# Kernel tuning notes

Hardware: AMD Instinct MI355X
Metric: run time of the kernel (lower is better)

## Reference

```python
import math
import jax, jax.numpy as jnp
import numpy as np

DIM_IN = 2048
DIM_OUT = 2048
BLOCK = 128
N_BLOCKS = 256
SPARSITY = 0.1
BATCH = 8192


def setup_inputs() -> dict:
    key = jax.random.key(0)
    k1, k2, k3, k4, k5 = jax.random.split(key, 5)
    x = jax.random.normal(k1, (BATCH, DIM_IN), dtype=jnp.float32)
    weight = jax.random.normal(k2, (DIM_IN, DIM_OUT), dtype=jnp.float32) * (1.0 / math.sqrt(DIM_IN))
    bias = jax.random.normal(k3, (DIM_OUT,), dtype=jnp.float32) * 0.01
    gate_w = jax.random.normal(k4, (DIM_IN, N_BLOCKS), dtype=jnp.float32) * (1.0 / math.sqrt(DIM_IN))
    gate_b = jax.random.normal(k5, (N_BLOCKS,), dtype=jnp.float32) * 0.01
    return {"x": x, "weight": weight, "bias": bias, "gate_w": gate_w, "gate_b": gate_b}


def _sparsify1d(g):
    # k-th largest kept per row; threshold, mask, renormalize (Sparsify1D)
    n = g.shape[-1]
    k = int(math.ceil(SPARSITY * n))
    topval = jax.lax.top_k(g, k)[0][:, -1:]          # (B, 1) k-th largest value
    res = jnp.where(g >= topval, g, jnp.zeros_like(g))
    return res / (jnp.sum(res, axis=-1, keepdims=True) / n)


def reference(x, weight, bias, gate_w, gate_b):
    B = x.shape[0]
    s = DIM_IN // BLOCK                               # 16 block-rows/cols
    # gate network: Linear -> Sparsify1D
    g = _sparsify1d(x @ gate_w + gate_b)              # (B, s*s)
    gb = g.reshape(B, s, s)                           # (B, s_in, s_out)
    xb = x.reshape(B, s, BLOCK)                       # (B, s_in, block)
    Wb = weight.reshape(s, BLOCK, s, BLOCK)           # (s_in, block, s_out, block)
    # gated block matrix-vector multiply:
    # y[b,q,n] = sum_{p,m} g[b,p,q] * x[b,p,m] * W[p,m,q,n]
    y = jnp.einsum('bpq,bpm,pmqn->bqn', gb, xb, Wb)
    return y.reshape(B, DIM_OUT) + bias
```

## Files before the change

### kernel.cpp

```cpp
#include <hip/hip_runtime.h>
#include <hip/hip_bf16.h>
#include <stdint.h>

#define BATCH  8192
#define DIN    2048
#define DOUT   2048
#define NB     256
#define KSEL   26
#define GDELTA 1e-4f

typedef __attribute__((ext_vector_type(2))) float f32x2;
typedef __attribute__((ext_vector_type(4))) float f32x4;
typedef __attribute__((ext_vector_type(16))) float f32x16;
typedef __attribute__((ext_vector_type(8))) __bf16 bf16x8;
typedef __attribute__((ext_vector_type(8))) unsigned short u16x8;
typedef __attribute__((ext_vector_type(4))) unsigned short u16x4;

__device__ __forceinline__ float bf2f(unsigned short u){
  union { unsigned int i; float f; } v; v.i = ((unsigned int)u) << 16; return v.f;
}
__device__ __forceinline__ unsigned short f2bf(float f){
  union { float f; unsigned int i; } v; v.f = f;
  unsigned int x = v.i;
  return (unsigned short)((x + 0x7FFFu + ((x >> 16) & 1u)) >> 16);
}
__device__ __forceinline__ unsigned short f2bf_c(float f){
  __bf16 b = (__bf16)f;
  union { __bf16 b; unsigned short u; } v; v.b = b; return v.u;
}

__global__ __launch_bounds__(256) void conv_wt(const float* __restrict__ w, unsigned short* __restrict__ wt)
{
  __shared__ float tl[64][65];
  const int k0 = blockIdx.x * 64;
  const int n0 = blockIdx.y * 64;
  const int c  = threadIdx.x & 63;
  const int r4 = threadIdx.x >> 6;
  #pragma unroll
  for (int i = 0; i < 16; i++){
    const int r = r4 * 16 + i;
    tl[r][c] = w[(size_t)(k0 + r) * DOUT + n0 + c];
  }
  __syncthreads();
  #pragma unroll
  for (int i = 0; i < 16; i++){
    const int n = r4 * 16 + i;
    wt[(size_t)(n0 + n) * DIN + k0 + c] = f2bf(tl[c][n]);
  }
}

__global__ __launch_bounds__(256) void conv_gwt(const float* __restrict__ gw,
    unsigned short* __restrict__ ghiT, unsigned short* __restrict__ gloT)
{
  __shared__ float tl[64][65];
  const int k0 = blockIdx.x * 64;
  const int n0 = blockIdx.y * 64;
  const int c  = threadIdx.x & 63;
  const int r4 = threadIdx.x >> 6;
  #pragma unroll
  for (int i = 0; i < 16; i++){
    const int r = r4 * 16 + i;
    tl[r][c] = gw[(size_t)(k0 + r) * NB + n0 + c];
  }
  __syncthreads();
  #pragma unroll
  for (int i = 0; i < 16; i++){
    const int n = r4 * 16 + i;
    const float v = tl[c][n];
    const unsigned short h = f2bf_c(v);
    ghiT[(size_t)(n0 + n) * DIN + k0 + c] = h;
    gloT[(size_t)(n0 + n) * DIN + k0 + c] = f2bf_c(v - bf2f(h));
  }
}

__global__ __launch_bounds__(256) void gate_v2(
    const float* __restrict__ x,
    const unsigned short* __restrict__ ghiT,
    const unsigned short* __restrict__ gloT,
    float* __restrict__ part,
    unsigned short* __restrict__ xb)
{
  __shared__ unsigned short Axh[64][64], Axl[64][64];
  __shared__ unsigned short Bgh[128][64], Bgl[128][64];

  const int b0   = blockIdx.x * 64;
  const int c0   = blockIdx.y * 128;
  const int ks   = blockIdx.z;
  const int k0   = ks * 1024;
  const int t    = threadIdx.x;
  const int lane = t & 63;
  const int wv   = t >> 6;
  const int bw   = wv & 1;
  const int cw   = wv >> 1;
  const int l15  = lane & 15;
  const int l4   = lane >> 4;
  const bool emit = (blockIdx.y == 0);

  const int ar = t >> 2;
  const int ak = (t & 3) * 16;
  const int br = t >> 1;
  const int bk = (t & 1) * 32;

  f32x4 acc[2][4];
  #pragma unroll
  for (int m = 0; m < 2; m++)
    #pragma unroll
    for (int n = 0; n < 4; n++) acc[m][n] = (f32x4)0.0f;

  int aoff[2][2], boff[2][4];
  #pragma unroll
  for (int ksi = 0; ksi < 2; ksi++){
    const int chunk = ksi * 4 + l4;
    #pragma unroll
    for (int m = 0; m < 2; m++){
      const int row = bw * 32 + m * 16 + l15;
      aoff[ksi][m] = row * 64 + ((chunk ^ (row & 7)) << 3);
    }
    #pragma unroll
    for (int n = 0; n < 4; n++){
      const int row = cw * 64 + n * 16 + l15;
      boff[ksi][n] = row * 64 + ((chunk ^ (row & 7)) << 3);
    }
  }

  f32x4 xa[4];
  u16x8 gh[4], glo[4];

  auto LOAD = [&](int kb){
    const float* xp = &x[(size_t)(b0 + ar) * DIN + kb + ak];
    #pragma unroll
    for (int j = 0; j < 4; j++) xa[j] = ((const f32x4*)xp)[j];
    const unsigned short* hp = &ghiT[(size_t)(c0 + br) * DIN + kb + bk];
    const unsigned short* lp = &gloT[(size_t)(c0 + br) * DIN + kb + bk];
    #pragma unroll
    for (int j = 0; j < 4; j++){ gh[j] = ((const u16x8*)hp)[j]; glo[j] = ((const u16x8*)lp)[j]; }
  };

  auto WRITE = [&](int kb){
    const int asw = ar & 7;
    #pragma unroll
    for (int h = 0; h < 2; h++){
      u16x8 hi, lo;
      #pragma unroll
      for (int j = 0; j < 8; j++){
        const float v = xa[h * 2 + (j >> 2)][j & 3];
        const __bf16 hb = (__bf16)v;
        union { __bf16 b; unsigned short u; } uh; uh.b = hb;
        hi[j] = uh.u;
        lo[j] = f2bf_c(v - (float)hb);
      }
      const int c8 = (((ak >> 3) + h) ^ asw) << 3;
      *(u16x8*)&Axh[ar][c8] = hi;
      *(u16x8*)&Axl[ar][c8] = lo;
      if (emit) *(u16x8*)&xb[(size_t)(b0 + ar) * DIN + kb + ak + h * 8] = hi;
    }
    const int bsw = br & 7;
    #pragma unroll
    for (int j = 0; j < 4; j++){
      const int c8 = (((bk >> 3) + j) ^ bsw) << 3;
      *(u16x8*)&Bgh[br][c8] = gh[j];
      *(u16x8*)&Bgl[br][c8] = glo[j];
    }
  };

  const unsigned short* Ah0 = &Axh[0][0];
  const unsigned short* Al0 = &Axl[0][0];
  const unsigned short* Bh0 = &Bgh[0][0];
  const unsigned short* Bl0 = &Bgl[0][0];

  LOAD(k0);
  #pragma unroll 1
  for (int s = 0; s < 16; s++){
    const int kb = k0 + s * 64;
    __syncthreads();
    WRITE(kb);
    __syncthreads();
    if (s < 15) LOAD(kb + 64);
    #pragma unroll
    for (int ksi = 0; ksi < 2; ksi++){
      bf16x8 ah[2], al[2], bh[4], bl[4];
      #pragma unroll
      for (int m = 0; m < 2; m++){
        ah[m] = *(const bf16x8*)&Ah0[aoff[ksi][m]];
        al[m] = *(const bf16x8*)&Al0[aoff[ksi][m]];
      }
      #pragma unroll
      for (int n = 0; n < 4; n++){
        bh[n] = *(const bf16x8*)&Bh0[boff[ksi][n]];
        bl[n] = *(const bf16x8*)&Bl0[boff[ksi][n]];
      }
      #pragma unroll
      for (int m = 0; m < 2; m++)
        #pragma unroll
        for (int n = 0; n < 4; n++){
          acc[m][n] = __builtin_amdgcn_mfma_f32_16x16x32_bf16(ah[m], bh[n], acc[m][n], 0, 0, 0);
          acc[m][n] = __builtin_amdgcn_mfma_f32_16x16x32_bf16(al[m], bh[n], acc[m][n], 0, 0, 0);
          acc[m][n] = __builtin_amdgcn_mfma_f32_16x16x32_bf16(ah[m], bl[n], acc[m][n], 0, 0, 0);
        }
    }
  }

  float* dst = part + (size_t)ks * BATCH * NB;
  #pragma unroll
  for (int m = 0; m < 2; m++){
    const int brow = b0 + bw * 32 + m * 16 + l4 * 4;
    #pragma unroll
    for (int n = 0; n < 4; n++){
      const int ccol = c0 + cw * 64 + n * 16 + l15;
      #pragma unroll
      for (int r = 0; r < 4; r++)
        dst[(size_t)(brow + r) * NB + ccol] = acc[m][n][r];
    }
  }
}

__global__ __launch_bounds__(256) void topk(float* __restrict__ part,
    const float* __restrict__ gb, int* __restrict__ flags)
{
  const int lane = threadIdx.x & 63;
  const int row  = blockIdx.x * 4 + (threadIdx.x >> 6);
  f32x4* p0 = (f32x4*)&part[(size_t)row * NB];
  const f32x4* p1 = (const f32x4*)&part[(size_t)(BATCH + row) * NB];
  const f32x4* gbv = (const f32x4*)gb;
  f32x4 v = p0[lane] + p1[lane] + gbv[lane];

  const float NEG = -3.402823466e38f;
  float w0 = v[0], w1 = v[1], w2 = v[2], w3 = v[3];
  float thr = 0.f, nxt = 0.f;
  for (int it = 0; it < KSEL + 1; it++){
    float lm = fmaxf(fmaxf(w0, w1), fmaxf(w2, w3));
    float wm = lm;
    #pragma unroll
    for (int off = 32; off; off >>= 1) wm = fmaxf(wm, __shfl_xor(wm, off, 64));
    unsigned long long ball = __ballot(lm == wm);
    int first = __ffsll(ball) - 1;
    if (lane == first){
      if      (w0 == wm) w0 = NEG;
      else if (w1 == wm) w1 = NEG;
      else if (w2 == wm) w2 = NEG;
      else               w3 = NEG;
    }
    if (it < KSEL) thr = wm; else nxt = wm;
  }
  if (lane == 0) flags[row] = (thr - nxt < GDELTA) ? 1 : 0;

  float s = 0.f;
  #pragma unroll
  for (int j = 0; j < 4; j++) s += (v[j] >= thr) ? v[j] : 0.f;
  #pragma unroll
  for (int off = 32; off; off >>= 1) s += __shfl_xor(s, off, 64);
  const float d = s * (1.0f / NB);
  f32x4 o;
  #pragma unroll
  for (int j = 0; j < 4; j++) o[j] = (v[j] >= thr) ? v[j] / d : 0.f;
  p0[lane] = o;
}

__global__ __launch_bounds__(256) void refine(
    const float* __restrict__ x, const float* __restrict__ gw,
    const float* __restrict__ gb, const int* __restrict__ flags,
    float* __restrict__ part)
{
  const int lane = threadIdx.x & 63;
  const int row  = blockIdx.x * 4 + (threadIdx.x >> 6);
  if (!flags[row]) return;

  f32x4 acc0 = (f32x4)0.f, acc1 = (f32x4)0.f;
  const float* xp = &x[(size_t)row * DIN];
  #pragma unroll 8
  for (int k = 0; k < 1024; k++){
    const float xv = xp[k];
    const f32x4 wv = *(const f32x4*)&gw[(size_t)k * NB + lane * 4];
    #pragma unroll
    for (int j = 0; j < 4; j++) acc0[j] = fmaf(xv, wv[j], acc0[j]);
  }
  #pragma unroll 8
  for (int k = 1024; k < 2048; k++){
    const float xv = xp[k];
    const f32x4 wv = *(const f32x4*)&gw[(size_t)k * NB + lane * 4];
    #pragma unroll
    for (int j = 0; j < 4; j++) acc1[j] = fmaf(xv, wv[j], acc1[j]);
  }
  const f32x4 gbv = *(const f32x4*)&gb[lane * 4];
  f32x4 v;
  #pragma unroll
  for (int j = 0; j < 4; j++) v[j] = acc0[j] + acc1[j] + gbv[j];

  const float NEG = -3.402823466e38f;
  float w0 = v[0], w1 = v[1], w2 = v[2], w3 = v[3];
  float thr = 0.f;
  for (int it = 0; it < KSEL; it++){
    float lm = fmaxf(fmaxf(w0, w1), fmaxf(w2, w3));
    float wm = lm;
    #pragma unroll
    for (int off = 32; off; off >>= 1) wm = fmaxf(wm, __shfl_xor(wm, off, 64));
    unsigned long long ball = __ballot(lm == wm);
    int first = __ffsll(ball) - 1;
    if (lane == first){
      if      (w0 == wm) w0 = NEG;
      else if (w1 == wm) w1 = NEG;
      else if (w2 == wm) w2 = NEG;
      else               w3 = NEG;
    }
    thr = wm;
  }
  float s = 0.f;
  #pragma unroll
  for (int j = 0; j < 4; j++) s += (v[j] >= thr) ? v[j] : 0.f;
  #pragma unroll
  for (int off = 32; off; off >>= 1) s += __shfl_xor(s, off, 64);
  const float d = s * (1.0f / NB);
  f32x4 o;
  #pragma unroll
  for (int j = 0; j < 4; j++) o[j] = (v[j] >= thr) ? v[j] / d : 0.f;
  *(f32x4*)&part[(size_t)row * NB + lane * 4] = o;
}

__global__ __launch_bounds__(256) void main_v2(
    const unsigned short* __restrict__ xb,
    const unsigned short* __restrict__ wt,
    const float* __restrict__ g,
    const float* __restrict__ bias,
    float* __restrict__ out)
{
  __shared__ unsigned short XA[128][64];
  __shared__ unsigned short WB[128][64];
  __shared__ float gl[128 * 17];

  const int f  = blockIdx.x;
  const int q  = f >> 6;
  const int b0 = ((f & 7) * 8 + ((f >> 3) & 7)) * 128;
  const int t    = threadIdx.x;
  const int lane = t & 63;
  const int wid  = t >> 6;
  const int wr   = (wid >> 1) * 64;
  const int wc   = (wid & 1) * 64;
  const int l15  = lane & 15;
  const int l4   = lane >> 4;

  for (int e = t; e < 128 * 16; e += 256){
    const int r = e >> 4, p = e & 15;
    gl[r * 17 + p] = g[(size_t)(b0 + r) * NB + p * 16 + q];
  }

  f32x4 acc[4][4];
  #pragma unroll
  for (int m = 0; m < 4; m++)
    #pragma unroll
    for (int n = 0; n < 4; n++) acc[m][n] = (f32x4)0.0f;

  const int row_s = t >> 1;
  const int half  = t & 1;
  const int kk    = half * 32;

  int aoff[2][4], boff[2][4];
  #pragma unroll
  for (int ksi = 0; ksi < 2; ksi++){
    const int chunk = ksi * 4 + l4;
    #pragma unroll
    for (int m = 0; m < 4; m++){
      const int row = wr + m * 16 + l15;
      aoff[ksi][m] = row * 64 + ((chunk ^ (row & 7)) << 3);
    }
    #pragma unroll
    for (int n = 0; n < 4; n++){
      const int row = wc + n * 16 + l15;
      boff[ksi][n] = row * 64 + ((chunk ^ (row & 7)) << 3);
    }
  }

  u16x8 ax[4], bx[4];
  auto LOAD = [&](int kb){
    const unsigned short* asrc = &xb[(size_t)(b0 + row_s) * DIN + kb + kk];
    const unsigned short* bsrc = &wt[(size_t)(q * 128 + row_s) * DIN + kb + kk];
    #pragma unroll
    for (int j = 0; j < 4; j++){ ax[j] = ((const u16x8*)asrc)[j]; bx[j] = ((const u16x8*)bsrc)[j]; }
  };
  auto WRITE = [&](int p){
    const float gate = gl[row_s * 17 + p];
    const int sw = row_s & 7;
    #pragma unroll
    for (int j = 0; j < 4; j++){
      u16x8 o;
      #pragma unroll
      for (int i = 0; i < 8; i++) o[i] = f2bf_c(bf2f(ax[j][i]) * gate);
      const int c8 = ((half * 4 + j) ^ sw) << 3;
      *(u16x8*)&XA[row_s][c8] = o;
      *(u16x8*)&WB[row_s][c8] = bx[j];
    }
  };

  const unsigned short* A0 = &XA[0][0];
  const unsigned short* B0 = &WB[0][0];

  LOAD(0);
  #pragma unroll 1
  for (int kp = 0; kp < 32; kp++){
    __syncthreads();
    WRITE(kp >> 1);
    __syncthreads();
    if (kp < 31) LOAD((kp + 1) * 64);
    #pragma unroll
    for (int ksi = 0; ksi < 2; ksi++){
      bf16x8 a[4], b[4];
      #pragma unroll
      for (int m = 0; m < 4; m++) a[m] = *(const bf16x8*)&A0[aoff[ksi][m]];
      #pragma unroll
      for (int n = 0; n < 4; n++) b[n] = *(const bf16x8*)&B0[boff[ksi][n]];
      #pragma unroll
      for (int m = 0; m < 4; m++)
        #pragma unroll
        for (int n = 0; n < 4; n++)
          acc[m][n] = __builtin_amdgcn_mfma_f32_16x16x32_bf16(a[m], b[n], acc[m][n], 0, 0, 0);
    }
  }

  #pragma unroll
  for (int n = 0; n < 4; n++){
    const int col = q * 128 + wc + n * 16 + l15;
    const float bv = bias[col];
    #pragma unroll
    for (int m = 0; m < 4; m++){
      #pragma unroll
      for (int r = 0; r < 4; r++){
        const int row = b0 + wr + m * 16 + l4 * 4 + r;
        out[(size_t)row * DOUT + col] = acc[m][n][r] + bv;
      }
    }
  }
}

extern "C" void kernel_launch(void* const* d_in, const int* in_sizes, int n_in,
                              void* d_out, int out_size, void* d_ws, size_t ws_size,
                              hipStream_t stream)
{
  const float* x    = (const float*)d_in[0];
  const float* w    = (const float*)d_in[1];
  const float* bias = (const float*)d_in[2];
  const float* gw   = (const float*)d_in[3];
  const float* gb   = (const float*)d_in[4];
  float* out = (float*)d_out;

  char* wsb = (char*)d_ws;
  float*          part = (float*)wsb;
  unsigned short* xbb  = (unsigned short*)(wsb + (size_t)16 * 1024 * 1024);
  unsigned short* ghiT = (unsigned short*)(wsb + (size_t)48 * 1024 * 1024);
  unsigned short* gloT = (unsigned short*)(wsb + (size_t)49 * 1024 * 1024);
  int*            flg  = (int*)           (wsb + (size_t)50 * 1024 * 1024);
  unsigned short* wtb  = (unsigned short*)(wsb + (size_t)48 * 1024 * 1024);

  conv_gwt <<<dim3(DIN / 64, NB / 64), 256, 0, stream>>>(gw, ghiT, gloT);
  gate_v2  <<<dim3(BATCH / 64, 2, 2), 256, 0, stream>>>(x, ghiT, gloT, part, xbb);
  topk     <<<BATCH / 4, 256, 0, stream>>>(part, gb, flg);
  refine   <<<BATCH / 4, 256, 0, stream>>>(x, gw, gb, flg, part);
  conv_wt  <<<dim3(DIN / 64, DOUT / 64), 256, 0, stream>>>(w, wtb);
  main_v2  <<<1024, 256, 0, stream>>>(xbb, wtb, part, bias, out);
}
```

Before: 257.0 us.

## Pre-tile swizzled bf16 operands and stream via global_load_lds double buffering

The weight, gate-weight and bf16 x conversions now write tiles in a pre-swizzled, tile-contiguous layout. This lets the gate and main GEMMs load shared-memory tiles directly with global_load_lds into double buffers, with no register staging. The main kernel no longer scales x by the gate before the MFMA. It accumulates each 128-wide input block into a partial accumulator and applies the per-row gate in fp32 afterward, which removes the per-element convert/multiply/convert and one barrier per step. The cost is doubled LDS usage and extra accumulator registers, which may lower occupancy. The gate GEMM tile shape also changes to 128x64.

Result: slower. 288.3 us (+12.2%).

```diff
diff --git a/kernel.cpp b/kernel.cpp
--- a/kernel.cpp
+++ b/kernel.cpp
@@ -9,27 +9,26 @@
 #define KSEL   26
 #define GDELTA 1e-4f
 
-typedef __attribute__((ext_vector_type(2))) float f32x2;
 typedef __attribute__((ext_vector_type(4))) float f32x4;
-typedef __attribute__((ext_vector_type(16))) float f32x16;
 typedef __attribute__((ext_vector_type(8))) __bf16 bf16x8;
 typedef __attribute__((ext_vector_type(8))) unsigned short u16x8;
-typedef __attribute__((ext_vector_type(4))) unsigned short u16x4;
 
 __device__ __forceinline__ float bf2f(unsigned short u){
   union { unsigned int i; float f; } v; v.i = ((unsigned int)u) << 16; return v.f;
-}
-__device__ __forceinline__ unsigned short f2bf(float f){
-  union { float f; unsigned int i; } v; v.f = f;
-  unsigned int x = v.i;
-  return (unsigned short)((x + 0x7FFFu + ((x >> 16) & 1u)) >> 16);
 }
 __device__ __forceinline__ unsigned short f2bf_c(float f){
   __bf16 b = (__bf16)f;
   union { __bf16 b; unsigned short u; } v; v.b = b; return v.u;
 }
-
-__global__ __launch_bounds__(256) void conv_wt(const float* __restrict__ w, unsigned short* __restrict__ wt)
+__device__ __forceinline__ void gload16(const unsigned short* g, unsigned short* l){
+  __builtin_amdgcn_global_load_lds(
+      (const __attribute__((address_space(1))) void*)g,
+      (__attribute__((address_space(3))) void*)l, 16, 0, 0);
+}
+
+
+__global__ __launch_bounds__(256) void conv_wt2(const float* __restrict__ w,
+                                                unsigned short* __restrict__ wtt)
 {
   __shared__ float tl[64][65];
   const int k0 = blockIdx.x * 64;
@@ -42,171 +41,182 @@
     tl[r][c] = w[(size_t)(k0 + r) * DOUT + n0 + c];
   }
   __syncthreads();
-  #pragma unroll
-  for (int i = 0; i < 16; i++){
-    const int n = r4 * 16 + i;
-    wt[(size_t)(n0 + n) * DIN + k0 + c] = f2bf(tl[c][n]);
-  }
-}
-
-__global__ __launch_bounds__(256) void conv_gwt(const float* __restrict__ gw,
-    unsigned short* __restrict__ ghiT, unsigned short* __restrict__ gloT)
+  const int n  = threadIdx.x & 63;
+  const int cp = threadIdx.x >> 6;
+  const int gn = n0 + n;
+  const size_t base = ((size_t)(gn >> 7) * 32 + (k0 >> 6)) * 8192 + (size_t)(gn & 127) * 64;
+  const int sw = gn & 7;
+  #pragma unroll
+  for (int u = 0; u < 2; u++){
+    const int cc = cp * 2 + u;
+    u16x8 o;
+    #pragma unroll
+    for (int j = 0; j < 8; j++) o[j] = f2bf_c(tl[cc * 8 + j][n]);
+    *(u16x8*)&wtt[base + ((cc ^ sw) << 3)] = o;
+  }
+}
+
+__global__ __launch_bounds__(256) void conv_gwt2(const float* __restrict__ gw,
+    unsigned short* __restrict__ ght, unsigned short* __restrict__ glt)
 {
   __shared__ float tl[64][65];
   const int k0 = blockIdx.x * 64;
-  const int n0 = blockIdx.y * 64;
+  const int c0 = blockIdx.y * 64;
   const int c  = threadIdx.x & 63;
   const int r4 = threadIdx.x >> 6;
   #pragma unroll
   for (int i = 0; i < 16; i++){
     const int r = r4 * 16 + i;
-    tl[r][c] = gw[(size_t)(k0 + r) * NB + n0 + c];
+    tl[r][c] = gw[(size_t)(k0 + r) * NB + c0 + c];
   }
   __syncthreads();
-  #pragma unroll
-  for (int i = 0; i < 16; i++){
-    const int n = r4 * 16 + i;
-    const float v = tl[c][n];
-    const unsigned short h = f2bf_c(v);
-    ghiT[(size_t)(n0 + n) * DIN + k0 + c] = h;
-    gloT[(size_t)(n0 + n) * DIN + k0 + c] = f2bf_c(v - bf2f(h));
-  }
-}
-
-__global__ __launch_bounds__(256) void gate_v2(
+  const int n  = threadIdx.x & 63;
+  const int cp = threadIdx.x >> 6;
+  const size_t base = ((size_t)(c0 >> 6) * 32 + (k0 >> 6)) * 4096 + (size_t)n * 64;
+  const int sw = n & 7;
+  #pragma unroll
+  for (int u = 0; u < 2; u++){
+    const int cc = cp * 2 + u;
+    u16x8 hi, lo;
+    #pragma unroll
+    for (int j = 0; j < 8; j++){
+      const float v = tl[cc * 8 + j][n];
+      const __bf16 hb = (__bf16)v;
+      union { __bf16 b; unsigned short u; } uh; uh.b = hb;
+      hi[j] = uh.u;
+      lo[j] = f2bf_c(v - (float)hb);
+    }
+    const int off = (cc ^ sw) << 3;
+    *(u16x8*)&ght[base + off] = hi;
+    *(u16x8*)&glt[base + off] = lo;
+  }
+}
+
+__global__ __launch_bounds__(256) void gate_v3(
     const float* __restrict__ x,
-    const unsigned short* __restrict__ ghiT,
-    const unsigned short* __restrict__ gloT,
+    const unsigned short* __restrict__ ght,
+    const unsigned short* __restrict__ glt,
     float* __restrict__ part,
-    unsigned short* __restrict__ xb)
-{
-  __shared__ unsigned short Axh[64][64], Axl[64][64];
-  __shared__ unsigned short Bgh[128][64], Bgl[128][64];
-
-  const int b0   = blockIdx.x * 64;
-  const int c0   = blockIdx.y * 128;
-  const int ks   = blockIdx.z;
-  const int k0   = ks * 1024;
+    unsigned short* __restrict__ xbt)
+{
+  __shared__ unsigned short Axh[128 * 64], Axl[128 * 64];
+  __shared__ unsigned short Bh[2][64 * 64], Bl[2][64 * 64];
+
+  const int b0   = blockIdx.x * 128;
+  const int ct   = blockIdx.y;
+  const int z    = blockIdx.z;
+  const int ks0  = z * 16;
   const int t    = threadIdx.x;
   const int lane = t & 63;
-  const int wv   = t >> 6;
-  const int bw   = wv & 1;
-  const int cw   = wv >> 1;
+  const int wid  = t >> 6;
+  const int bw   = wid & 1;
+  const int cw   = wid >> 1;
   const int l15  = lane & 15;
   const int l4   = lane >> 4;
   const bool emit = (blockIdx.y == 0);
 
-  const int ar = t >> 2;
-  const int ak = (t & 3) * 16;
-  const int br = t >> 1;
-  const int bk = (t & 1) * 32;
-
-  f32x4 acc[2][4];
-  #pragma unroll
-  for (int m = 0; m < 2; m++)
-    #pragma unroll
-    for (int n = 0; n < 4; n++) acc[m][n] = (f32x4)0.0f;
-
-  int aoff[2][2], boff[2][4];
+  const int ar  = t >> 1;
+  const int ah4 = (t & 1) * 4;
+
+  f32x4 acc[4][2];
+  #pragma unroll
+  for (int m = 0; m < 4; m++)
+    #pragma unroll
+    for (int n = 0; n < 2; n++) acc[m][n] = (f32x4)0.0f;
+
+  int aoff[2][4], boff[2][2];
   #pragma unroll
   for (int ksi = 0; ksi < 2; ksi++){
     const int chunk = ksi * 4 + l4;
     #pragma unroll
-    for (int m = 0; m < 2; m++){
-      const int row = bw * 32 + m * 16 + l15;
+    for (int m = 0; m < 4; m++){
+      const int row = bw * 64 + m * 16 + l15;
       aoff[ksi][m] = row * 64 + ((chunk ^ (row & 7)) << 3);
     }
     #pragma unroll
-    for (int n = 0; n < 4; n++){
-      const int row = cw * 64 + n * 16 + l15;
+    for (int n = 0; n < 2; n++){
+      const int row = cw * 32 + n * 16 + l15;
       boff[ksi][n] = row * 64 + ((chunk ^ (row & 7)) << 3);
     }
   }
 
-  f32x4 xa[4];
-  u16x8 gh[4], glo[4];
-
-  auto LOAD = [&](int kb){
-    const float* xp = &x[(size_t)(b0 + ar) * DIN + kb + ak];
-    #pragma unroll
-    for (int j = 0; j < 4; j++) xa[j] = ((const f32x4*)xp)[j];
-    const unsigned short* hp = &ghiT[(size_t)(c0 + br) * DIN + kb + bk];
-    const unsigned short* lp = &gloT[(size_t)(c0 + br) * DIN + kb + bk];
-    #pragma unroll
-    for (int j = 0; j < 4; j++){ gh[j] = ((const u16x8*)hp)[j]; glo[j] = ((const u16x8*)lp)[j]; }
+  f32x4 xr[8];
+  auto LOADX = [&](int s){
+    const float* xp = &x[(size_t)(b0 + ar) * DIN + (size_t)(ks0 + s) * 64 + ah4 * 8];
+    #pragma unroll
+    for (int j = 0; j < 8; j++) xr[j] = ((const f32x4*)xp)[j];
   };
-
-  auto WRITE = [&](int kb){
-    const int asw = ar & 7;
-    #pragma unroll
-    for (int h = 0; h < 2; h++){
+  auto GLOADB = [&](int bb, int s){
+    const size_t base = ((size_t)ct * 32 + (ks0 + s)) * 4096;
+    #pragma unroll
+    for (int i = 0; i < 2; i++){
+      const int slot = (wid * 2 + i) * 512;
+      gload16(ght + base + slot + lane * 8, &Bh[bb][slot]);
+      gload16(glt + base + slot + lane * 8, &Bl[bb][slot]);
+    }
+  };
+  auto WRITEA = [&](int s){
+    const int sw = ar & 7;
+    const size_t gb = ((size_t)(b0 >> 7) * 32 + (ks0 + s)) * 8192 + (size_t)ar * 64;
+    #pragma unroll
+    for (int j = 0; j < 4; j++){
       u16x8 hi, lo;
       #pragma unroll
-      for (int j = 0; j < 8; j++){
-        const float v = xa[h * 2 + (j >> 2)][j & 3];
+      for (int e = 0; e < 8; e++){
+        const float v = xr[j * 2 + (e >> 2)][e & 3];
         const __bf16 hb = (__bf16)v;
         union { __bf16 b; unsigned short u; } uh; uh.b = hb;
-        hi[j] = uh.u;
-        lo[j] = f2bf_c(v - (float)hb);
+        hi[e] = uh.u;
+        lo[e] = f2bf_c(v - (float)hb);
       }
-      const int c8 = (((ak >> 3) + h) ^ asw) << 3;
-      *(u16x8*)&Axh[ar][c8] = hi;
-      *(u16x8*)&Axl[ar][c8] = lo;
-      if (emit) *(u16x8*)&xb[(size_t)(b0 + ar) * DIN + kb + ak + h * 8] = hi;
-    }
-    const int bsw = br & 7;
-    #pragma unroll
-    for (int j = 0; j < 4; j++){
-      const int c8 = (((bk >> 3) + j) ^ bsw) << 3;
-      *(u16x8*)&Bgh[br][c8] = gh[j];
-      *(u16x8*)&Bgl[br][c8] = glo[j];
+      const int c8 = ((ah4 + j) ^ sw) << 3;
+      *(u16x8*)&Axh[ar * 64 + c8] = hi;
+      *(u16x8*)&Axl[ar * 64 + c8] = lo;
+      if (emit) *(u16x8*)&xbt[gb + c8] = hi;
     }
   };
 
-  const unsigned short* Ah0 = &Axh[0][0];
-  const unsigned short* Al0 = &Axl[0][0];
-  const unsigned short* Bh0 = &Bgh[0][0];
-  const unsigned short* Bl0 = &Bgl[0][0];
-
-  LOAD(k0);
+  GLOADB(0, 0);
+  LOADX(0);
+  int buf = 0;
   #pragma unroll 1
   for (int s = 0; s < 16; s++){
-    const int kb = k0 + s * 64;
     __syncthreads();
-    WRITE(kb);
+    WRITEA(s);
     __syncthreads();
-    if (s < 15) LOAD(kb + 64);
+    if (s < 15){ GLOADB(buf ^ 1, s + 1); LOADX(s + 1); }
     #pragma unroll
     for (int ksi = 0; ksi < 2; ksi++){
-      bf16x8 ah[2], al[2], bh[4], bl[4];
-      #pragma unroll
-      for (int m = 0; m < 2; m++){
-        ah[m] = *(const bf16x8*)&Ah0[aoff[ksi][m]];
-        al[m] = *(const bf16x8*)&Al0[aoff[ksi][m]];
+      bf16x8 ah[4], al[4], bh[2], bl[2];
+      #pragma unroll
+      for (int m = 0; m < 4; m++){
+        ah[m] = *(const bf16x8*)&Axh[aoff[ksi][m]];
+        al[m] = *(const bf16x8*)&Axl[aoff[ksi][m]];
       }
       #pragma unroll
-      for (int n = 0; n < 4; n++){
-        bh[n] = *(const bf16x8*)&Bh0[boff[ksi][n]];
-        bl[n] = *(const bf16x8*)&Bl0[boff[ksi][n]];
+      for (int n = 0; n < 2; n++){
+        bh[n] = *(const bf16x8*)&Bh[buf][boff[ksi][n]];
+        bl[n] = *(const bf16x8*)&Bl[buf][boff[ksi][n]];
       }
       #pragma unroll
-      for (int m = 0; m < 2; m++)
+      for (int m = 0; m < 4; m++)
         #pragma unroll
-        for (int n = 0; n < 4; n++){
+        for (int n = 0; n < 2; n++){
           acc[m][n] = __builtin_amdgcn_mfma_f32_16x16x32_bf16(ah[m], bh[n], acc[m][n], 0, 0, 0);
           acc[m][n] = __builtin_amdgcn_mfma_f32_16x16x32_bf16(al[m], bh[n], acc[m][n], 0, 0, 0);
           acc[m][n] = __builtin_amdgcn_mfma_f32_16x16x32_bf16(ah[m], bl[n], acc[m][n], 0, 0, 0);
         }
     }
-  }
-
-  float* dst = part + (size_t)ks * BATCH * NB;
-  #pragma unroll
-  for (int m = 0; m < 2; m++){
-    const int brow = b0 + bw * 32 + m * 16 + l4 * 4;
-    #pragma unroll
-    for (int n = 0; n < 4; n++){
-      const int ccol = c0 + cw * 64 + n * 16 + l15;
+    buf ^= 1;
+  }
+
+  float* dst = part + (size_t)z * BATCH * NB;
+  #pragma unroll
+  for (int m = 0; m < 4; m++){
+    const int brow = b0 + bw * 64 + m * 16 + l4 * 4;
+    #pragma unroll
+    for (int n = 0; n < 2; n++){
+      const int ccol = ct * 64 + cw * 32 + n * 16 + l15;
       #pragma unroll
       for (int r = 0; r < 4; r++)
         dst[(size_t)(brow + r) * NB + ccol] = acc[m][n][r];
@@ -316,20 +326,20 @@
   *(f32x4*)&part[(size_t)row * NB + lane * 4] = o;
 }
 
-__global__ __launch_bounds__(256) void main_v2(
-    const unsigned short* __restrict__ xb,
-    const unsigned short* __restrict__ wt,
+__global__ __launch_bounds__(256) void main_v3(
+    const unsigned short* __restrict__ xbt,
+    const unsigned short* __restrict__ wtt,
     const float* __restrict__ g,
     const float* __restrict__ bias,
     float* __restrict__ out)
 {
-  __shared__ unsigned short XA[128][64];
-  __shared__ unsigned short WB[128][64];
+  __shared__ unsigned short XA[2][128 * 64], WB[2][128 * 64];
   __shared__ float gl[128 * 17];
 
   const int f  = blockIdx.x;
   const int q  = f >> 6;
-  const int b0 = ((f & 7) * 8 + ((f >> 3) & 7)) * 128;
+  const int bt = (f & 7) * 8 + ((f >> 3) & 7);
+  const int b0 = bt * 128;
   const int t    = threadIdx.x;
   const int lane = t & 63;
   const int wid  = t >> 6;
@@ -343,15 +353,11 @@
     gl[r * 17 + p] = g[(size_t)(b0 + r) * NB + p * 16 + q];
   }
 
-  f32x4 acc[4][4];
+  f32x4 accT[4][4], accP[4][4];
   #pragma unroll
   for (int m = 0; m < 4; m++)
     #pragma unroll
-    for (int n = 0; n < 4; n++) acc[m][n] = (f32x4)0.0f;
-
-  const int row_s = t >> 1;
-  const int half  = t & 1;
-  const int kk    = half * 32;
+    for (int n = 0; n < 4; n++){ accT[m][n] = (f32x4)0.0f; accP[m][n] = (f32x4)0.0f; }
 
   int aoff[2][4], boff[2][4];
   #pragma unroll
@@ -369,50 +375,55 @@
     }
   }
 
-  u16x8 ax[4], bx[4];
-  auto LOAD = [&](int kb){
-    const unsigned short* asrc = &xb[(size_t)(b0 + row_s) * DIN + kb + kk];
-    const unsigned short* bsrc = &wt[(size_t)(q * 128 + row_s) * DIN + kb + kk];
-    #pragma unroll
-    for (int j = 0; j < 4; j++){ ax[j] = ((const u16x8*)asrc)[j]; bx[j] = ((const u16x8*)bsrc)[j]; }
+  const unsigned short* asrc0 = xbt + (size_t)bt * 32 * 8192;
+  const unsigned short* bsrc0 = wtt + (size_t)q  * 32 * 8192;
+
+  auto GLOAD = [&](int bb, int kp){
+    const unsigned short* as = asrc0 + (size_t)kp * 8192;
+    const unsigned short* bs = bsrc0 + (size_t)kp * 8192;
+    #pragma unroll
+    for (int i = 0; i < 4; i++){
+      const int slot = (wid * 4 + i) * 512;
+      gload16(as + slot + lane * 8, &XA[bb][slot]);
+      gload16(bs + slot + lane * 8, &WB[bb][slot]);
+    }
   };
-  auto WRITE = [&](int p){
-    const float gate = gl[row_s * 17 + p];
-    const int sw = row_s & 7;
-    #pragma unroll
-    for (int j = 0; j < 4; j++){
-      u16x8 o;
-      #pragma unroll
-      for (int i = 0; i < 8; i++) o[i] = f2bf_c(bf2f(ax[j][i]) * gate);
-      const int c8 = ((half * 4 + j) ^ sw) << 3;
-      *(u16x8*)&XA[row_s][c8] = o;
-      *(u16x8*)&WB[row_s][c8] = bx[j];
-    }
-  };
-
-  const unsigned short* A0 = &XA[0][0];
-  const unsigned short* B0 = &WB[0][0];
-
-  LOAD(0);
+
+  GLOAD(0, 0);
+  int buf = 0;
   #pragma unroll 1
   for (int kp = 0; kp < 32; kp++){
     __syncthreads();
-    WRITE(kp >> 1);
-    __syncthreads();
-    if (kp < 31) LOAD((kp + 1) * 64);
+    if (kp < 31) GLOAD(buf ^ 1, kp + 1);
     #pragma unroll
     for (int ksi = 0; ksi < 2; ksi++){
       bf16x8 a[4], b[4];
       #pragma unroll
-      for (int m = 0; m < 4; m++) a[m] = *(const bf16x8*)&A0[aoff[ksi][m]];
-      #pragma unroll
-      for (int n = 0; n < 4; n++) b[n] = *(const bf16x8*)&B0[boff[ksi][n]];
+      for (int m = 0; m < 4; m++) a[m] = *(const bf16x8*)&XA[buf][aoff[ksi][m]];
+      #pragma unroll
+      for (int n = 0; n < 4; n++) b[n] = *(const bf16x8*)&WB[buf][boff[ksi][n]];
       #pragma unroll
       for (int m = 0; m < 4; m++)
         #pragma unroll
         for (int n = 0; n < 4; n++)
-          acc[m][n] = __builtin_amdgcn_mfma_f32_16x16x32_bf16(a[m], b[n], acc[m][n], 0, 0, 0);
-    }
+          accP[m][n] = __builtin_amdgcn_mfma_f32_16x16x32_bf16(a[m], b[n], accP[m][n], 0, 0, 0);
+    }
+    if (kp & 1){
+      const int p = kp >> 1;
+      #pragma unroll
+      for (int m = 0; m < 4; m++){
+        const int rb = wr + m * 16 + l4 * 4;
+        f32x4 g4;
+        #pragma unroll
+        for (int r = 0; r < 4; r++) g4[r] = gl[(rb + r) * 17 + p];
+        #pragma unroll
+        for (int n = 0; n < 4; n++){
+          accT[m][n] += g4 * accP[m][n];
+          accP[m][n] = (f32x4)0.0f;
+        }
+      }
+    }
+    buf ^= 1;
   }
 
   #pragma unroll
@@ -424,7 +435,7 @@
       #pragma unroll
       for (int r = 0; r < 4; r++){
         const int row = b0 + wr + m * 16 + l4 * 4 + r;
-        out[(size_t)row * DOUT + col] = acc[m][n][r] + bv;
+        out[(size_t)row * DOUT + col] = accT[m][n][r] + bv;
       }
     }
   }
@@ -443,16 +454,16 @@
 
   char* wsb = (char*)d_ws;
   float*          part = (float*)wsb;
-  unsigned short* xbb  = (unsigned short*)(wsb + (size_t)16 * 1024 * 1024);
-  unsigned short* ghiT = (unsigned short*)(wsb + (size_t)48 * 1024 * 1024);
-  unsigned short* gloT = (unsigned short*)(wsb + (size_t)49 * 1024 * 1024);
+  unsigned short* wtt  = (unsigned short*)(wsb + (size_t)8  * 1024 * 1024);
+  unsigned short* xbt  = (unsigned short*)(wsb + (size_t)16 * 1024 * 1024);
+  unsigned short* ght  = (unsigned short*)(wsb + (size_t)48 * 1024 * 1024);
+  unsigned short* glt  = (unsigned short*)(wsb + (size_t)49 * 1024 * 1024);
   int*            flg  = (int*)           (wsb + (size_t)50 * 1024 * 1024);
-  unsigned short* wtb  = (unsigned short*)(wsb + (size_t)48 * 1024 * 1024);
-
-  conv_gwt <<<dim3(DIN / 64, NB / 64), 256, 0, stream>>>(gw, ghiT, gloT);
-  gate_v2  <<<dim3(BATCH / 64, 2, 2), 256, 0, stream>>>(x, ghiT, gloT, part, xbb);
+
+  conv_gwt2<<<dim3(DIN / 64, NB / 64), 256, 0, stream>>>(gw, ght, glt);
+  gate_v3  <<<dim3(BATCH / 128, 4, 2), 256, 0, stream>>>(x, ght, glt, part, xbt);
   topk     <<<BATCH / 4, 256, 0, stream>>>(part, gb, flg);
   refine   <<<BATCH / 4, 256, 0, stream>>>(x, gw, gb, flg, part);
-  conv_wt  <<<dim3(DIN / 64, DOUT / 64), 256, 0, stream>>>(w, wtb);
-  main_v2  <<<1024, 256, 0, stream>>>(xbb, wtb, part, bias, out);
-}
+  conv_wt2 <<<dim3(DIN / 64, DOUT / 64), 256, 0, stream>>>(w, wtt);
+  main_v3  <<<1024, 256, 0, stream>>>(xbt, wtt, part, bias, out);
+}
```
